# Kernel tuning notes

Hardware: AMD Instinct MI355X
Metric: run time of the kernel (lower is better)

## Reference

```python
import jax, jax.numpy as jnp
import numpy as np
from jax import lax

RADIUS = 0.2
K = 32
EPS = 1e-5  # torch BatchNorm default eps

B, N, M, C = 16, 4096, 1024, 64


def setup_inputs() -> dict:
    key = jax.random.key(0)
    ks = jax.random.split(key, 8)
    src_x = jax.random.normal(ks[0], (B, N, C), dtype=jnp.float32)
    src_xyz = jax.random.uniform(ks[1], (B, N, 3), dtype=jnp.float32)
    xyz = jax.random.uniform(ks[2], (B, M, 3), dtype=jnp.float32)
    w1 = jax.random.normal(ks[3], (64, C + 3), dtype=jnp.float32) * 0.05
    w2 = jax.random.normal(ks[4], (128, 64), dtype=jnp.float32) * 0.05
    w3 = jax.random.normal(ks[5], (256, 128), dtype=jnp.float32) * 0.05
    return {
        "src_x": src_x, "src_xyz": src_xyz, "xyz": xyz,
        "w1": w1, "g1": jnp.ones(64), "b1": jnp.zeros(64),
        "w2": w2, "g2": jnp.ones(128), "b2": jnp.zeros(128),
        "w3": w3, "gl": jnp.ones(256), "bl": jnp.zeros(256),
    }


def _ball_query(src_xyz, xyz):
    # squared distances [B, M, N]
    d2 = jnp.sum((xyz[:, :, None, :] - src_xyz[:, None, :, :]) ** 2, axis=-1)
    n = src_xyz.shape[1]
    col = jnp.arange(n, dtype=jnp.int32)
    # encode: in-ball points keep their index, others get sentinel n
    score = jnp.where(d2 <= RADIUS * RADIUS, col, n)
    neg_top, _ = lax.top_k(-score, K)        # k smallest scores (first-k in index order)
    gidx = -neg_top                          # [B, M, K]
    first = gidx[..., :1]
    first = jnp.where(first >= n, 0, first)  # no neighbor at all -> 0 (degenerate)
    gidx = jnp.where(gidx >= n, first, gidx)  # pad slots repeat first neighbor
    return gidx


def _gather(src, gidx):
    # src [B, N, D], gidx [B, M, K] -> [B, M, K, D]
    b, m, k = gidx.shape
    out = jnp.take_along_axis(src, gidx.reshape(b, m * k, 1), axis=1)
    return out.reshape(b, m, k, src.shape[-1])


def _bn(x, g, b, axes):
    # training-mode batch norm over given axes, per last-dim channel (biased var)
    mean = jnp.mean(x, axis=axes, keepdims=True)
    var = jnp.mean((x - mean) ** 2, axis=axes, keepdims=True)
    return (x - mean) * lax.rsqrt(var + EPS) * g + b


def _gelu(x):
    return jax.nn.gelu(x, approximate=False)  # torch nn.GELU default (erf)


def reference(src_x, src_xyz, xyz, w1, g1, b1, w2, g2, b2, w3, gl, bl):
    gidx = _ball_query(src_xyz, xyz)                 # [B, M, K]
    grouped_xyz = _gather(src_xyz, gidx)             # [B, M, K, 3]
    centered = grouped_xyz - xyz[:, :, None, :]
    grouped_x = _gather(src_x, gidx)                 # [B, M, K, C]
    feat = jnp.concatenate([centered, grouped_x], axis=-1)  # [B, M, K, C+3]

    h = _gelu(_bn(jnp.einsum("bmkc,oc->bmko", feat, w1), g1, b1, (0, 1, 2)))
    h = _gelu(_bn(jnp.einsum("bmkc,oc->bmko", h, w2), g2, b2, (0, 1, 2)))
    h = jnp.einsum("bmkc,oc->bmko", h, w3)
    h = jnp.max(h, axis=2)                           # max over k neighbors -> [B, M, 256]
    return _gelu(_bn(h, gl, bl, (0, 1)))             # BatchNorm1d over (batch, points)
```

## Files before the change

kernel.cpp:

```cpp
#include <hip/hip_runtime.h>
#include <math.h>

#define BB 16
#define NN 4096
#define MM 1024
#define KNN 32
#define R2 0.04f
#define EPSV 1e-5f
#define S1f ((float)(BB * MM * KNN))
#define S3f ((float)(BB * MM))

typedef __attribute__((ext_vector_type(8))) short short8;
typedef __attribute__((ext_vector_type(4))) short short4v;
typedef __attribute__((ext_vector_type(4))) float f32x4;

__device__ __forceinline__ short f2b(float x) {
    union { float f; unsigned u; } v; v.f = x;
    unsigned r = v.u + 0x7fffu + ((v.u >> 16) & 1u);
    return (short)(r >> 16);
}
__device__ __forceinline__ float b2f(short s) {
    union { unsigned u; float f; } v; v.u = ((unsigned)(unsigned short)s) << 16;
    return v.f;
}
__device__ __forceinline__ float gelu_t(float x) {
    float u = 0.7978845608f * x * (1.f + 0.044715f * x * x);
    float e = __expf(2.f * u);
    float r = __builtin_amdgcn_rcpf(e + 1.f);
    return x - x * r;
}
__device__ __forceinline__ float gelu_e(float x) {
    return 0.5f * x * (1.f + erff(x * 0.7071067811865475f));
}
__device__ __forceinline__ f32x4 zero4() { f32x4 z = {0.f, 0.f, 0.f, 0.f}; return z; }
__device__ __forceinline__ f32x4 mfma(short8 a, short8 b, f32x4 c) {
    return __builtin_amdgcn_mfma_f32_16x16x32_bf16(a, b, c, 0, 0, 0);
}
__device__ __forceinline__ short8 pack8(f32x4 a, f32x4 b) {
    short8 r;
    r[0] = f2b(a[0]); r[1] = f2b(a[1]); r[2] = f2b(a[2]); r[3] = f2b(a[3]);
    r[4] = f2b(b[0]); r[5] = f2b(b[1]); r[6] = f2b(b[2]); r[7] = f2b(b[3]);
    return r;
}

__global__ __launch_bounds__(256) void k_ballquery(const float* __restrict__ src_xyz,
                                                   const float* __restrict__ xyz,
                                                   int* __restrict__ gidx) {
    __shared__ float sx[NN], sy[NN], sz[NN];
    int t = threadIdx.x;
    int lane = t & 63, w = t >> 6;
    int q0 = blockIdx.x * 16;
    int b = q0 >> 10;
    const float* sp = src_xyz + (size_t)b * NN * 3;
    for (int i = t; i < NN * 3; i += 256) {
        float v = sp[i];
        int j = i / 3, d = i - j * 3;
        if (d == 0) sx[j] = v;
        else if (d == 1) sy[j] = v;
        else sz[j] = v;
    }
    __syncthreads();
#pragma unroll
    for (int qi = 0; qi < 4; ++qi) {
        int q = q0 + w * 4 + qi;
        int m = q & 1023;
        float qx = xyz[((size_t)b * MM + m) * 3 + 0];
        float qy = xyz[((size_t)b * MM + m) * 3 + 1];
        float qz = xyz[((size_t)b * MM + m) * 3 + 2];
        int* outp = gidx + (size_t)q * KNN;
        int cnt = 0, firstj = -1;
        for (int j0 = 0; j0 < NN && cnt < KNN; j0 += 64) {
            int j = j0 + lane;
            float dx = qx - sx[j];
            float dy = qy - sy[j];
            float dz = qz - sz[j];
            bool hit = (dx * dx + dy * dy + dz * dz) <= R2;
            unsigned long long mask = __ballot(hit);
            if (hit) {
                int rank = cnt + __popcll(mask & ((1ull << lane) - 1ull));
                if (rank < KNN) outp[rank] = j;
            }
            if (firstj < 0 && mask != 0ull) firstj = j0 + __ffsll((long long)mask) - 1;
            cnt += __popcll(mask);
        }
        if (cnt < KNN) {
            int fj = (firstj < 0) ? 0 : firstj;
            for (int k = cnt + lane; k < KNN; k += 64) outp[k] = fj;
        }
    }
}

__global__ __launch_bounds__(256) void k_prep(const float* __restrict__ src_x,
                                              const float* __restrict__ w1,
                                              const float* __restrict__ w2,
                                              const float* __restrict__ w3,
                                              short* __restrict__ src_xb,
                                              short* __restrict__ w1p,
                                              short* __restrict__ w2p,
                                              short* __restrict__ w3p) {
    int i = blockIdx.x * 256 + threadIdx.x;
    if (i < 524288) {
        const f32x4* p = (const f32x4*)(src_x + (size_t)i * 8);
        *(short8*)(src_xb + (size_t)i * 8) = pack8(p[0], p[1]);
    } else {
        int j = i - 524288;
        if (j < 6144) {
            int e = j & 7, lane = (j >> 3) & 63, idx = j >> 9;
            int kf = idx >> 2, nf = idx & 3;
            int ln = lane & 15, qq = lane >> 4;
            int n = nf * 16 + ln, k = kf * 32 + qq * 8 + e;
            float v = 0.f;
            if (k < 64) v = w1[n * 67 + 3 + k];
            else if (k < 67) v = w1[n * 67 + (k - 64)];
            w1p[j] = f2b(v);
        } else if (j < 14336) {
            int j2 = j - 6144;
            int e = j2 & 7, lane = (j2 >> 3) & 63, idx = j2 >> 9;
            int kf = idx >> 3, nf = idx & 7;
            int ln = lane & 15, qq = lane >> 4;
            w2p[j2] = f2b(w2[(nf * 16 + ln) * 64 + kf * 32 + qq * 8 + e]);
        } else if (j < 47104) {
            int j2 = j - 14336;
            int e = j2 & 7, lane = (j2 >> 3) & 63, idx = j2 >> 9;
            int nf = idx & 3, kf = (idx >> 2) & 3, nc = idx >> 4;
            int ln = lane & 15, qq = lane >> 4;
            w3p[j2] = f2b(w3[(size_t)(nc * 64 + nf * 16 + ln) * 128 + kf * 32 + qq * 8 + e]);
        }
    }
}

#define GATHER_WAVE(R)                                                                  \
    {                                                                                   \
        if (lane < 8) { short4v z4 = {0, 0, 0, 0};                                      \
            *(short4v*)((R) + 2304 + lane * 4) = z4; }                                  \
        int r = lane >> 1, hf = lane & 1;                                               \
        int jdx = gidx[(size_t)g * KNN + r];                                            \
        const short8* sp = (const short8*)(src_xb + ((size_t)b * NN + jdx) * 64 + hf * 32); \
        *(short8*)((R) + r * 72 + hf * 32) = sp[0];                                     \
        *(short8*)((R) + r * 72 + hf * 32 + 8) = sp[1];                                 \
        *(short8*)((R) + r * 72 + hf * 32 + 16) = sp[2];                                \
        *(short8*)((R) + r * 72 + hf * 32 + 24) = sp[3];                                \
        if (hf == 0) {                                                                  \
            const float* spp = src_xyz + ((size_t)b * NN + jdx) * 3;                    \
            short4v z;                                                                  \
            z[0] = f2b(spp[0] - qx); z[1] = f2b(spp[1] - qy);                           \
            z[2] = f2b(spp[2] - qz); z[3] = 0;                                          \
            *(short4v*)((R) + r * 72 + 64) = z;                                         \
            short4v z0 = {0, 0, 0, 0};                                                  \
            *(short4v*)((R) + r * 72 + 68) = z0;                                        \
        }                                                                               \
    }

#define BN1_SCALES                                                                      \
    if (t < 64) {                                                                       \
        float s = 0.f, sq = 0.f;                                                        \
        _Pragma("unroll")                                                               \
        for (int r = 0; r < 8; ++r) { s += stats1[r * 128 + t]; sq += stats1[r * 128 + 64 + t]; } \
        float mu = s * (1.f / S1f);                                                     \
        float var = sq * (1.f / S1f) - mu * mu;                                         \
        float rs = rsqrtf(var + EPSV);                                                  \
        float sc = g1[t] * rs;                                                          \
        sc1L[t] = sc;                                                                   \
        sh1L[t] = b1[t] - mu * sc;                                                      \
    }

#define L1_SWAPPED(R, acc1)                                                             \
    short8 bAct[2][3];                                                                  \
    _Pragma("unroll")                                                                   \
    for (int sf = 0; sf < 2; ++sf)                                                      \
        _Pragma("unroll")                                                               \
        for (int kf = 0; kf < 3; ++kf)                                                  \
            bAct[sf][kf] = *(const short8*)((R) + (sf * 16 + ln) * 72 + kf * 32 + qq * 8); \
    _Pragma("unroll")                                                                   \
    for (int sf = 0; sf < 2; ++sf)                                                      \
        _Pragma("unroll")                                                               \
        for (int nf = 0; nf < 4; ++nf) acc1[sf][nf] = zero4();                          \
    _Pragma("unroll")                                                                   \
    for (int kf = 0; kf < 3; ++kf)                                                      \
        _Pragma("unroll")                                                               \
        for (int nf = 0; nf < 4; ++nf) {                                                \
            short8 aW = *(const short8*)(w1p + (((kf * 4 + nf) * 64) + lane) * 8);      \
            acc1[0][nf] = mfma(aW, bAct[0][kf], acc1[0][nf]);                           \
            acc1[1][nf] = mfma(aW, bAct[1][kf], acc1[1][nf]);                           \
        }

__global__ __launch_bounds__(256, 6) void k_s1(const int* __restrict__ gidx,
                                               const float* __restrict__ src_xyz,
                                               const float* __restrict__ xyz,
                                               const short* __restrict__ src_xb,
                                               const short* __restrict__ w1p,
                                               float* __restrict__ stats1) {
    __shared__ short wbuf[4][2336];
    __shared__ float redS[256], redQ[256];
    int t = threadIdx.x, lane = t & 63, w = t >> 6, ln = lane & 15, qq = lane >> 4;
    int g = blockIdx.x * 4 + w, b = g >> 10, m = g & 1023;
    float qx = xyz[((size_t)b * MM + m) * 3 + 0];
    float qy = xyz[((size_t)b * MM + m) * 3 + 1];
    float qz = xyz[((size_t)b * MM + m) * 3 + 2];
    short* R = wbuf[w];
    GATHER_WAVE(R)
    short8 aAct[2][3];
#pragma unroll
    for (int sf = 0; sf < 2; ++sf)
#pragma unroll
        for (int kf = 0; kf < 3; ++kf)
            aAct[sf][kf] = *(const short8*)(R + (sf * 16 + ln) * 72 + kf * 32 + qq * 8);
    f32x4 acc1[2][4];
#pragma unroll
    for (int sf = 0; sf < 2; ++sf)
#pragma unroll
        for (int nf = 0; nf < 4; ++nf) acc1[sf][nf] = zero4();
#pragma unroll
    for (int kf = 0; kf < 3; ++kf)
#pragma unroll
        for (int nf = 0; nf < 4; ++nf) {
            short8 bW = *(const short8*)(w1p + (((kf * 4 + nf) * 64) + lane) * 8);
            acc1[0][nf] = mfma(aAct[0][kf], bW, acc1[0][nf]);
            acc1[1][nf] = mfma(aAct[1][kf], bW, acc1[1][nf]);
        }
#pragma unroll
    for (int nf = 0; nf < 4; ++nf) {
        f32x4 sv, qv;
#pragma unroll
        for (int jj = 0; jj < 4; ++jj) {
            float a0 = acc1[0][nf][jj], a1 = acc1[1][nf][jj];
            sv[jj] = a0 + a1; qv[jj] = a0 * a0 + a1 * a1;
        }
        float s = (sv[0] + sv[1]) + (sv[2] + sv[3]);
        float q = (qv[0] + qv[1]) + (qv[2] + qv[3]);
        s += __shfl_xor(s, 16); s += __shfl_xor(s, 32);
        q += __shfl_xor(q, 16); q += __shfl_xor(q, 32);
        if (qq == 0) { redS[w * 64 + nf * 16 + ln] = s; redQ[w * 64 + nf * 16 + ln] = q; }
    }
    __syncthreads();
    if (t < 64) {
        float s = redS[t] + redS[64 + t] + redS[128 + t] + redS[192 + t];
        float q = redQ[t] + redQ[64 + t] + redQ[128 + t] + redQ[192 + t];
        float* st = stats1 + (blockIdx.x & 7) * 128;
        atomicAdd(&st[t], s);
        atomicAdd(&st[64 + t], q);
    }
}

__global__ __launch_bounds__(256, 4) void k_s2(const int* __restrict__ gidx,
                                               const float* __restrict__ src_xyz,
                                               const float* __restrict__ xyz,
                                               const short* __restrict__ src_xb,
                                               const short* __restrict__ w1p,
                                               const short* __restrict__ w2p,
                                               const float* __restrict__ g1,
                                               const float* __restrict__ b1,
                                               const float* __restrict__ stats1,
                                               float* __restrict__ stats2,
                                               short* __restrict__ h2p) {
    __shared__ short wbuf[4][2336];
    __shared__ float sc1L[64], sh1L[64];
    __shared__ float redS[512], redQ[512];
    int t = threadIdx.x, lane = t & 63, w = t >> 6, ln = lane & 15, qq = lane >> 4;
    int g = blockIdx.x * 4 + w, b = g >> 10, m = g & 1023;
    float qx = xyz[((size_t)b * MM + m) * 3 + 0];
    float qy = xyz[((size_t)b * MM + m) * 3 + 1];
    float qz = xyz[((size_t)b * MM + m) * 3 + 2];
    short* R = wbuf[w];
    GATHER_WAVE(R)
    BN1_SCALES
    f32x4 acc1[2][4];
    L1_SWAPPED(R, acc1)
    __syncthreads();
#pragma unroll
    for (int sf = 0; sf < 2; ++sf)
#pragma unroll
        for (int nf = 0; nf < 4; ++nf) {
            int c0 = nf * 16 + qq * 4;
            f32x4 sc = *(const f32x4*)(sc1L + c0);
            f32x4 sh = *(const f32x4*)(sh1L + c0);
            short4v sv;
#pragma unroll
            for (int jj = 0; jj < 4; ++jj)
                sv[jj] = f2b(gelu_t(acc1[sf][nf][jj] * sc[jj] + sh[jj]));
            *(short4v*)(R + (sf * 16 + ln) * 72 + c0) = sv;
        }
    short8 bh1[2][2];
#pragma unroll
    for (int sf = 0; sf < 2; ++sf)
#pragma unroll
        for (int kf = 0; kf < 2; ++kf)
            bh1[sf][kf] = *(const short8*)(R + (sf * 16 + ln) * 72 + kf * 32 + qq * 8);
    short* hb2 = h2p + (size_t)g * 4096;
#pragma unroll
    for (int hh2 = 0; hh2 < 2; ++hh2) {
        f32x4 acc2[2][4];
#pragma unroll
        for (int sf = 0; sf < 2; ++sf)
#pragma unroll
            for (int nfl = 0; nfl < 4; ++nfl) acc2[sf][nfl] = zero4();
#pragma unroll
        for (int kf = 0; kf < 2; ++kf)
#pragma unroll
            for (int nfl = 0; nfl < 4; ++nfl) {
                int nf = hh2 * 4 + nfl;
                short8 aW = *(const short8*)(w2p + (((kf * 8 + nf) * 64) + lane) * 8);
                acc2[0][nfl] = mfma(aW, bh1[0][kf], acc2[0][nfl]);
                acc2[1][nfl] = mfma(aW, bh1[1][kf], acc2[1][nfl]);
            }
#pragma unroll
        for (int sf = 0; sf < 2; ++sf)
#pragma unroll
            for (int nfl = 0; nfl < 4; ++nfl) {
                int c0 = nfl * 16 + qq * 4;
                short4v sv;
#pragma unroll
                for (int jj = 0; jj < 4; ++jj) sv[jj] = f2b(acc2[sf][nfl][jj]);
                *(short4v*)(R + (sf * 16 + ln) * 72 + c0) = sv;
            }
#pragma unroll
        for (int sf = 0; sf < 2; ++sf)
#pragma unroll
            for (int kfl = 0; kfl < 2; ++kfl) {
                short8 fr = *(const short8*)(R + (sf * 16 + ln) * 72 + kfl * 32 + qq * 8);
                *(short8*)(hb2 + ((sf * 4 + hh2 * 2 + kfl) * 64 + lane) * 8) = fr;
            }
#pragma unroll
        for (int nfl = 0; nfl < 4; ++nfl) {
            f32x4 s, q;
#pragma unroll
            for (int jj = 0; jj < 4; ++jj) {
                float a0 = acc2[0][nfl][jj], a1 = acc2[1][nfl][jj];
                s[jj] = a0 + a1; q[jj] = a0 * a0 + a1 * a1;
            }
#pragma unroll
            for (int d = 1; d < 16; d <<= 1) {
#pragma unroll
                for (int jj = 0; jj < 4; ++jj) {
                    s[jj] += __shfl_xor(s[jj], d);
                    q[jj] += __shfl_xor(q[jj], d);
                }
            }
            if (ln == 0) {
                *(f32x4*)(redS + w * 128 + (hh2 * 4 + nfl) * 16 + qq * 4) = s;
                *(f32x4*)(redQ + w * 128 + (hh2 * 4 + nfl) * 16 + qq * 4) = q;
            }
        }
    }
    __syncthreads();
    if (t < 128) {
        float s = redS[t] + redS[128 + t] + redS[256 + t] + redS[384 + t];
        float q = redQ[t] + redQ[128 + t] + redQ[256 + t] + redQ[384 + t];
        float* st = stats2 + (blockIdx.x & 7) * 256;
        atomicAdd(&st[t], s);
        atomicAdd(&st[128 + t], q);
    }
}

__global__ __launch_bounds__(256, 4) void k3(const short* __restrict__ h2p,
                                             const short* __restrict__ w3p,
                                             const float* __restrict__ g2,
                                             const float* __restrict__ b2,
                                             const float* __restrict__ stats2,
                                             float* __restrict__ stats3,
                                             float* __restrict__ out) {
    __shared__ float sc2L[128], sh2L[128];
    __shared__ float mxS[4][256];
    int t = threadIdx.x, lane = t & 63, w = t >> 6, ln = lane & 15, qq = lane >> 4;
    int g = blockIdx.x * 4 + w;
    const short* hbp = h2p + (size_t)g * 4096;
    short8 hv[2][4];
#pragma unroll
    for (int sf = 0; sf < 2; ++sf)
#pragma unroll
        for (int kf = 0; kf < 4; ++kf)
            hv[sf][kf] = *(const short8*)(hbp + ((sf * 4 + kf) * 64 + lane) * 8);
    if (t < 128) {
        float s = 0.f, sq = 0.f;
#pragma unroll
        for (int r = 0; r < 8; ++r) { s += stats2[r * 256 + t]; sq += stats2[r * 256 + 128 + t]; }
        float mu = s * (1.f / S1f);
        float var = sq * (1.f / S1f) - mu * mu;
        float rs = rsqrtf(var + EPSV);
        float sc = g2[t] * rs;
        sc2L[t] = sc;
        sh2L[t] = b2[t] - mu * sc;
    }
    __syncthreads();
#pragma unroll
    for (int sf = 0; sf < 2; ++sf)
#pragma unroll
        for (int kf = 0; kf < 4; ++kf) {
            int c0 = kf * 32 + qq * 8;
            f32x4 sa = *(const f32x4*)(sc2L + c0);
            f32x4 sb = *(const f32x4*)(sc2L + c0 + 4);
            f32x4 ha = *(const f32x4*)(sh2L + c0);
            f32x4 hbv = *(const f32x4*)(sh2L + c0 + 4);
            short8 r = hv[sf][kf];
            short8 o;
#pragma unroll
            for (int e = 0; e < 4; ++e)
                o[e] = f2b(gelu_t(b2f(r[e]) * sa[e] + ha[e]));
#pragma unroll
            for (int e = 0; e < 4; ++e)
                o[e + 4] = f2b(gelu_t(b2f(r[e + 4]) * sb[e] + hbv[e]));
            hv[sf][kf] = o;
        }
#pragma unroll
    for (int nc = 0; nc < 4; ++nc) {
        f32x4 acc3[2][4];
#pragma unroll
        for (int sf = 0; sf < 2; ++sf)
#pragma unroll
            for (int nf = 0; nf < 4; ++nf) acc3[sf][nf] = zero4();
#pragma unroll
        for (int kf = 0; kf < 4; ++kf)
#pragma unroll
            for (int nf = 0; nf < 4; ++nf) {
                short8 bW = *(const short8*)(w3p + (((nc * 4 + kf) * 4 + nf) * 64 + lane) * 8);
                acc3[0][nf] = mfma(hv[0][kf], bW, acc3[0][nf]);
                acc3[1][nf] = mfma(hv[1][kf], bW, acc3[1][nf]);
            }
#pragma unroll
        for (int nf = 0; nf < 4; ++nf) {
            f32x4 v0 = acc3[0][nf], v1 = acc3[1][nf];
            float m0 = fmaxf(fmaxf(v0[0], v0[1]), fmaxf(v0[2], v0[3]));
            float m1 = fmaxf(fmaxf(v1[0], v1[1]), fmaxf(v1[2], v1[3]));
            float mm = fmaxf(m0, m1);
            mm = fmaxf(mm, __shfl_xor(mm, 16));
            mm = fmaxf(mm, __shfl_xor(mm, 32));
            if (qq == 0) {
                out[(size_t)g * 256 + nc * 64 + nf * 16 + ln] = mm;
                mxS[w][nc * 64 + nf * 16 + ln] = mm;
            }
        }
    }
    __syncthreads();
    {
        float a0 = mxS[0][t], a1 = mxS[1][t], a2 = mxS[2][t], a3v = mxS[3][t];
        float s = a0 + a1 + a2 + a3v;
        float q = a0 * a0 + a1 * a1 + a2 * a2 + a3v * a3v;
        float* st = stats3 + (blockIdx.x & 7) * 512;
        atomicAdd(&st[t], s);
        atomicAdd(&st[256 + t], q);
    }
}

__global__ __launch_bounds__(256) void k_bn3(float* __restrict__ out,
                                             const float* __restrict__ stats3,
                                             const float* __restrict__ gl,
                                             const float* __restrict__ bl) {
    int i = blockIdx.x * 256 + threadIdx.x;
    int o = i & 255;
    float s = 0.f, q = 0.f;
#pragma unroll
    for (int r = 0; r < 8; ++r) { s += stats3[r * 512 + o]; q += stats3[r * 512 + 256 + o]; }
    float mu = s * (1.f / S3f);
    float var = q * (1.f / S3f) - mu * mu;
    float rs = rsqrtf(var + EPSV);
    float x = out[i];
    out[i] = gelu_e((x - mu) * rs * gl[o] + bl[o]);
}

extern "C" void kernel_launch(void* const* d_in, const int* in_sizes, int n_in,
                              void* d_out, int out_size, void* d_ws, size_t ws_size,
                              hipStream_t stream) {
    const float* src_x   = (const float*)d_in[0];
    const float* src_xyz = (const float*)d_in[1];
    const float* xyz     = (const float*)d_in[2];
    const float* w1      = (const float*)d_in[3];
    const float* g1      = (const float*)d_in[4];
    const float* b1      = (const float*)d_in[5];
    const float* w2      = (const float*)d_in[6];
    const float* g2      = (const float*)d_in[7];
    const float* b2      = (const float*)d_in[8];
    const float* w3      = (const float*)d_in[9];
    const float* gl      = (const float*)d_in[10];
    const float* bl      = (const float*)d_in[11];
    float* out = (float*)d_out;

    int* gidx = (int*)d_ws;
    float* statsF = (float*)(gidx + BB * MM * KNN);
    float* stats1 = statsF;
    float* stats2 = statsF + 1024;
    float* stats3 = statsF + 3072;
    short* wb = (short*)(statsF + 7168);
    short* w1p = wb;
    short* w2p = wb + 6144;
    short* w3p = wb + 14336;
    short* src_xb = wb + 47104;
    short* h2p = (short*)((char*)d_ws + (size_t)(16u << 20));

    hipMemsetAsync(statsF, 0, 7168 * sizeof(float), stream);
    k_prep<<<2232, 256, 0, stream>>>(src_x, w1, w2, w3, src_xb, w1p, w2p, w3p);
    k_ballquery<<<(BB * MM) / 16, 256, 0, stream>>>(src_xyz, xyz, gidx);
    k_s1<<<(BB * MM) / 4, 256, 0, stream>>>(gidx, src_xyz, xyz, src_xb, w1p, stats1);
    k_s2<<<(BB * MM) / 4, 256, 0, stream>>>(gidx, src_xyz, xyz, src_xb, w1p, w2p, g1, b1,
                                            stats1, stats2, h2p);
    k3<<<(BB * MM) / 4, 256, 0, stream>>>(h2p, w3p, g2, b2, stats2, stats3, out);
    k_bn3<<<BB * MM, 256, 0, stream>>>(out, stats3, gl, bl);
}
```

Baseline: 231.6 us.

## Store layer-1 pre-BN activations in bf16 instead of regathering and recomputing

New measurement: 240.1 us. +3.6%, slower.

```diff
diff --git a/kernel.cpp b/kernel.cpp
--- a/kernel.cpp
+++ b/kernel.cpp
@@ -184,12 +184,30 @@
             acc1[1][nf] = mfma(aW, bAct[1][kf], acc1[1][nf]);                           \
         }
 
+#define H1_DECODE(R, hv)                                                                \
+    _Pragma("unroll")                                                                   \
+    for (int i = 0; i < 4; ++i) {                                                       \
+        int sf_ = i >> 1, pr_ = i & 1;                                                  \
+        _Pragma("unroll")                                                               \
+        for (int hh = 0; hh < 2; ++hh) {                                                \
+            int c0_ = (2 * pr_ + hh) * 16 + qq * 4;                                     \
+            f32x4 sc = *(const f32x4*)(sc1L + c0_);                                     \
+            f32x4 sh = *(const f32x4*)(sh1L + c0_);                                     \
+            short4v sv;                                                                 \
+            _Pragma("unroll")                                                           \
+            for (int jj = 0; jj < 4; ++jj)                                              \
+                sv[jj] = f2b(gelu_t(b2f(hv[i][hh * 4 + jj]) * sc[jj] + sh[jj]));        \
+            *(short4v*)((R) + (sf_ * 16 + ln) * 72 + c0_) = sv;                         \
+        }                                                                               \
+    }
+
 __global__ __launch_bounds__(256, 6) void k_s1(const int* __restrict__ gidx,
                                                const float* __restrict__ src_xyz,
                                                const float* __restrict__ xyz,
                                                const short* __restrict__ src_xb,
                                                const short* __restrict__ w1p,
-                                               float* __restrict__ stats1) {
+                                               float* __restrict__ stats1,
+                                               short* __restrict__ h1p) {
     __shared__ short wbuf[4][2336];
     __shared__ float redS[256], redQ[256];
     int t = threadIdx.x, lane = t & 63, w = t >> 6, ln = lane & 15, qq = lane >> 4;
@@ -199,38 +217,36 @@
     float qz = xyz[((size_t)b * MM + m) * 3 + 2];
     short* R = wbuf[w];
     GATHER_WAVE(R)
-    short8 aAct[2][3];
-#pragma unroll
-    for (int sf = 0; sf < 2; ++sf)
-#pragma unroll
-        for (int kf = 0; kf < 3; ++kf)
-            aAct[sf][kf] = *(const short8*)(R + (sf * 16 + ln) * 72 + kf * 32 + qq * 8);
     f32x4 acc1[2][4];
-#pragma unroll
-    for (int sf = 0; sf < 2; ++sf)
-#pragma unroll
-        for (int nf = 0; nf < 4; ++nf) acc1[sf][nf] = zero4();
-#pragma unroll
-    for (int kf = 0; kf < 3; ++kf)
-#pragma unroll
-        for (int nf = 0; nf < 4; ++nf) {
-            short8 bW = *(const short8*)(w1p + (((kf * 4 + nf) * 64) + lane) * 8);
-            acc1[0][nf] = mfma(aAct[0][kf], bW, acc1[0][nf]);
-            acc1[1][nf] = mfma(aAct[1][kf], bW, acc1[1][nf]);
-        }
+    L1_SWAPPED(R, acc1)
+    {
+        short* hb = h1p + (size_t)g * 2048;
+#pragma unroll
+        for (int i = 0; i < 4; ++i) {
+            int sf = i >> 1, p = i & 1;
+            *(short8*)(hb + (i * 64 + lane) * 8) = pack8(acc1[sf][2 * p], acc1[sf][2 * p + 1]);
+        }
+    }
 #pragma unroll
     for (int nf = 0; nf < 4; ++nf) {
-        f32x4 sv, qv;
+        f32x4 s, q;
 #pragma unroll
         for (int jj = 0; jj < 4; ++jj) {
             float a0 = acc1[0][nf][jj], a1 = acc1[1][nf][jj];
-            sv[jj] = a0 + a1; qv[jj] = a0 * a0 + a1 * a1;
-        }
-        float s = (sv[0] + sv[1]) + (sv[2] + sv[3]);
-        float q = (qv[0] + qv[1]) + (qv[2] + qv[3]);
-        s += __shfl_xor(s, 16); s += __shfl_xor(s, 32);
-        q += __shfl_xor(q, 16); q += __shfl_xor(q, 32);
-        if (qq == 0) { redS[w * 64 + nf * 16 + ln] = s; redQ[w * 64 + nf * 16 + ln] = q; }
+            s[jj] = a0 + a1; q[jj] = a0 * a0 + a1 * a1;
+        }
+#pragma unroll
+        for (int d = 1; d < 16; d <<= 1) {
+#pragma unroll
+            for (int jj = 0; jj < 4; ++jj) {
+                s[jj] += __shfl_xor(s[jj], d);
+                q[jj] += __shfl_xor(q[jj], d);
+            }
+        }
+        if (ln == 0) {
+            *(f32x4*)(redS + w * 64 + nf * 16 + qq * 4) = s;
+            *(f32x4*)(redQ + w * 64 + nf * 16 + qq * 4) = q;
+        }
     }
     __syncthreads();
     if (t < 64) {
@@ -242,44 +258,26 @@
     }
 }
 
-__global__ __launch_bounds__(256, 4) void k_s2(const int* __restrict__ gidx,
-                                               const float* __restrict__ src_xyz,
-                                               const float* __restrict__ xyz,
-                                               const short* __restrict__ src_xb,
-                                               const short* __restrict__ w1p,
-                                               const short* __restrict__ w2p,
-                                               const float* __restrict__ g1,
-                                               const float* __restrict__ b1,
-                                               const float* __restrict__ stats1,
-                                               float* __restrict__ stats2,
-                                               short* __restrict__ h2p) {
+__global__ __launch_bounds__(256, 4) void k_s2f(const short* __restrict__ h1p,
+                                                const short* __restrict__ w2p,
+                                                const float* __restrict__ g1,
+                                                const float* __restrict__ b1,
+                                                const float* __restrict__ stats1,
+                                                float* __restrict__ stats2,
+                                                short* __restrict__ h2p) {
     __shared__ short wbuf[4][2336];
     __shared__ float sc1L[64], sh1L[64];
     __shared__ float redS[512], redQ[512];
     int t = threadIdx.x, lane = t & 63, w = t >> 6, ln = lane & 15, qq = lane >> 4;
-    int g = blockIdx.x * 4 + w, b = g >> 10, m = g & 1023;
-    float qx = xyz[((size_t)b * MM + m) * 3 + 0];
-    float qy = xyz[((size_t)b * MM + m) * 3 + 1];
-    float qz = xyz[((size_t)b * MM + m) * 3 + 2];
+    int g = blockIdx.x * 4 + w;
+    const short* hb = h1p + (size_t)g * 2048;
+    short8 hv[4];
+#pragma unroll
+    for (int i = 0; i < 4; ++i) hv[i] = *(const short8*)(hb + (i * 64 + lane) * 8);
+    BN1_SCALES
+    __syncthreads();
     short* R = wbuf[w];
-    GATHER_WAVE(R)
-    BN1_SCALES
-    f32x4 acc1[2][4];
-    L1_SWAPPED(R, acc1)
-    __syncthreads();
-#pragma unroll
-    for (int sf = 0; sf < 2; ++sf)
-#pragma unroll
-        for (int nf = 0; nf < 4; ++nf) {
-            int c0 = nf * 16 + qq * 4;
-            f32x4 sc = *(const f32x4*)(sc1L + c0);
-            f32x4 sh = *(const f32x4*)(sh1L + c0);
-            short4v sv;
-#pragma unroll
-            for (int jj = 0; jj < 4; ++jj)
-                sv[jj] = f2b(gelu_t(acc1[sf][nf][jj] * sc[jj] + sh[jj]));
-            *(short4v*)(R + (sf * 16 + ln) * 72 + c0) = sv;
-        }
+    H1_DECODE(R, hv)
     short8 bh1[2][2];
 #pragma unroll
     for (int sf = 0; sf < 2; ++sf)
@@ -484,14 +482,14 @@
     short* w2p = wb + 6144;
     short* w3p = wb + 14336;
     short* src_xb = wb + 47104;
-    short* h2p = (short*)((char*)d_ws + (size_t)(16u << 20));
+    short* h1p = (short*)((char*)d_ws + ((size_t)16u << 20));
+    short* h2p = (short*)((char*)d_ws + ((size_t)80u << 20));
 
     hipMemsetAsync(statsF, 0, 7168 * sizeof(float), stream);
     k_prep<<<2232, 256, 0, stream>>>(src_x, w1, w2, w3, src_xb, w1p, w2p, w3p);
     k_ballquery<<<(BB * MM) / 16, 256, 0, stream>>>(src_xyz, xyz, gidx);
-    k_s1<<<(BB * MM) / 4, 256, 0, stream>>>(gidx, src_xyz, xyz, src_xb, w1p, stats1);
-    k_s2<<<(BB * MM) / 4, 256, 0, stream>>>(gidx, src_xyz, xyz, src_xb, w1p, w2p, g1, b1,
-                                            stats1, stats2, h2p);
+    k_s1<<<(BB * MM) / 4, 256, 0, stream>>>(gidx, src_xyz, xyz, src_xb, w1p, stats1, h1p);
+    k_s2f<<<(BB * MM) / 4, 256, 0, stream>>>(h1p, w2p, g1, b1, stats1, stats2, h2p);
     k3<<<(BB * MM) / 4, 256, 0, stream>>>(h2p, w3p, g2, b2, stats2, stats3, out);
     k_bn3<<<BB * MM, 256, 0, stream>>>(out, stats3, gl, bl);
 }
```
